# Optimization experiments

Hardware: AMD Instinct MI355X
Metric: run time of the kernel (lower is better)

The kernel has to match this reference:

```python
import jax, jax.numpy as jnp
import numpy as np

B, C, H, W = 4, 64, 128, 128
NUM_HEAD = 1
SCALE = (C // NUM_HEAD) ** (-0.5)


def setup_inputs():
    key = jax.random.key(0)
    ks = jax.random.split(key, 32)
    def nrm(k, shape, s=0.05):
        return jax.random.normal(k, shape, jnp.float32) * s
    inp = {"x": jax.random.normal(ks[0], (B, C, H, W), jnp.float32)}
    i = 1
    for wn, bn in [("Wq", "bq"), ("Wk", "bk"), ("Wv", "bv"), ("Wl", "bl"), ("Wo", "bo"), ("Wp", "bp")]:
        inp[wn] = nrm(ks[i], (C, C)); i += 1
        inp[bn] = nrm(ks[i], (C,)); i += 1
    inp["sch_dw"] = nrm(ks[i], (C, 1, 5, 1)); i += 1
    inp["sch_dwb"] = nrm(ks[i], (C,)); i += 1
    inp["sch_pw"] = nrm(ks[i], (C, C, 1, 1)); i += 1
    inp["sch_pwb"] = nrm(ks[i], (C,)); i += 1
    inp["scv_dw"] = nrm(ks[i], (C, 1, 1, 5)); i += 1
    inp["scv_dwb"] = nrm(ks[i], (C,)); i += 1
    inp["scv_pw"] = nrm(ks[i], (C, C, 1, 1)); i += 1
    inp["scv_pwb"] = nrm(ks[i], (C,)); i += 1
    inp["convh_w"] = nrm(ks[i], (C, C, 1, 1)); i += 1
    inp["convh_b"] = nrm(ks[i], (C,)); i += 1
    inp["dsc_dw"] = nrm(ks[i], (C, 1, 3, 3)); i += 1
    inp["dsc_dwb"] = nrm(ks[i], (C,)); i += 1
    inp["dsc_pw"] = nrm(ks[i], (C, C, 1, 1)); i += 1
    inp["dsc_pwb"] = nrm(ks[i], (C,)); i += 1
    inp["ln_g"] = jnp.ones((C,), jnp.float32)
    inp["ln_b"] = jnp.zeros((C,), jnp.float32)
    return inp


def _linear(x, w, b):  # x [B,N,C], w [C,C] (torch Linear convention: y = x @ w.T + b)
    return x @ w.T + b


def _dwconv(x, w, b, pad):  # depthwise: x [B,C,H,W], w [C,1,kh,kw]
    y = jax.lax.conv_general_dilated(x, w, (1, 1), [(pad[0], pad[0]), (pad[1], pad[1])],
                                     dimension_numbers=("NCHW", "OIHW", "NCHW"),
                                     feature_group_count=x.shape[1])
    return y + b[None, :, None, None]


def _pwconv(x, w, b):  # 1x1 conv: w [Co,Ci,1,1]
    return jnp.einsum("bchw,oc->bohw", x, w[:, :, 0, 0]) + b[None, :, None, None]


def _attn(q, k, v):  # [B,N,C] each; dense NxN softmax attention
    a = jax.nn.softmax(jnp.einsum("bnc,bmc->bnm", q, k) * SCALE, axis=-1)
    return jnp.einsum("bnm,bmc->bnc", a, v)


def _up2_bilinear(x):  # bilinear, scale 2, align_corners=True
    Bb, Cc, Hh, Ww = x.shape
    def coords(n):
        s = jnp.linspace(0.0, n - 1.0, 2 * n)
        i0 = jnp.floor(s).astype(jnp.int32)
        i1 = jnp.minimum(i0 + 1, n - 1)
        return i0, i1, (s - i0).astype(x.dtype)
    y0, y1, wy = coords(Hh)
    x0, x1, wx = coords(Ww)
    r = x[:, :, y0, :] * (1.0 - wy)[None, None, :, None] + x[:, :, y1, :] * wy[None, None, :, None]
    return r[:, :, :, x0] * (1.0 - wx) + r[:, :, :, x1] * wx


def _forward(x, Wq, bq, Wk, bk, Wv, bv, Wl, bl, Wo, bo, Wp, bp,
             sch_dw, sch_dwb, sch_pw, sch_pwb, scv_dw, scv_dwb, scv_pw, scv_pwb,
             convh_w, convh_b, dsc_dw, dsc_dwb, dsc_pw, dsc_pwb, ln_g, ln_b):
    Bb, Cc, Hh, Ww = x.shape
    # AvgPool2d(2,2)
    xp = x.reshape(Bb, Cc, Hh // 2, 2, Ww // 2, 2).mean((3, 5))
    Hp, Wp_ = Hh // 2, Ww // 2
    N = Hp * Wp_
    # forward_lpg: GAP-gated self-attention producing low-freq prompt
    gap = xp.mean((2, 3), keepdims=True)
    xg = (gap * xp).reshape(Bb, Cc, N).transpose(0, 2, 1)  # [B,N,C]
    q = _linear(xg, Wq, bq); k = _linear(xg, Wk, bk); v = _linear(xg, Wv, bv)
    prompt_l = _linear(_attn(q, k, v), Wl, bl).transpose(0, 2, 1).reshape(Bb, Cc, Hp, Wp_)
    # forward_hpg: separable strip-conv branches -> high-freq prompt
    x_h = _pwconv(jax.nn.gelu(_dwconv(xp, sch_dw, sch_dwb, (2, 0)), approximate=False), sch_pw, sch_pwb)
    x_v = _pwconv(jax.nn.gelu(_dwconv(xp, scv_dw, scv_dwb, (0, 2)), approximate=False), scv_pw, scv_pwb)
    prompt_h = _pwconv(x_h + x_v, convh_w, convh_b)
    # forward_pgc: cross-attention Q=high, K=low, V=linear(x)
    x_V = _linear(xp.reshape(Bb, Cc, N).transpose(0, 2, 1), Wo, bo)
    x_K = prompt_l.reshape(Bb, Cc, N).transpose(0, 2, 1)
    x_Q = prompt_h.reshape(Bb, Cc, N).transpose(0, 2, 1)
    prompt = _attn(x_Q, x_K, x_V)
    prompt = _linear(prompt, Wp, bp) + x_V
    # LayerNorm over channel dim
    mu = prompt.mean(-1, keepdims=True)
    var = jnp.mean((prompt - mu) ** 2, axis=-1, keepdims=True)
    p_norm = (prompt - mu) / jnp.sqrt(var + 1e-5) * ln_g + ln_b
    p_norm = p_norm.transpose(0, 2, 1).reshape(Bb, Cc, Hp, Wp_)
    # dsc: depthwise 3x3 -> GELU -> 1x1, residual
    out = _pwconv(jax.nn.gelu(_dwconv(p_norm, dsc_dw, dsc_dwb, (1, 1)), approximate=False), dsc_pw, dsc_pwb) + p_norm
    return _up2_bilinear(out)


def reference(x, Wq, bq, Wk, bk, Wv, bv, Wl, bl, Wo, bo, Wp, bp,
              sch_dw, sch_dwb, sch_pw, sch_pwb, scv_dw, scv_dwb, scv_pw, scv_pwb,
              convh_w, convh_b, dsc_dw, dsc_dwb, dsc_pw, dsc_pwb, ln_g, ln_b):
    return _forward(x, Wq, bq, Wk, bk, Wv, bv, Wl, bl, Wo, bo, Wp, bp,
                    sch_dw, sch_dwb, sch_pw, sch_pwb, scv_dw, scv_dwb, scv_pw, scv_pwb,
                    convh_w, convh_b, dsc_dw, dsc_dwb, dsc_pw, dsc_pwb, ln_g, ln_b)
```

## Files before the change

kernel.cpp:

```cpp
#include <hip/hip_runtime.h>
#include <math.h>

#define Bn 4
#define Cn 64
#define Np 4096
#define NSPLIT 4
#define SCALE2 0.18033688011112042f

typedef unsigned short ushort_t;
typedef __attribute__((ext_vector_type(4))) float f32x4;
typedef __attribute__((ext_vector_type(8))) short bf16x8;
typedef __attribute__((ext_vector_type(4))) short bf16x4;

__device__ __forceinline__ float gelu_exact(float x) {
    return 0.5f * x * (1.0f + erff(x * 0.70710678118654752440f));
}
__device__ __forceinline__ ushort_t f2bf(float f) {
    unsigned int u = __float_as_uint(f);
    u += 0x7fffu + ((u >> 16) & 1u);
    return (ushort_t)(u >> 16);
}
__device__ __forceinline__ ushort_t f2bf_tr(float f) {
    return (ushort_t)(__float_as_uint(f) >> 16);
}
__device__ __forceinline__ float bf2f(ushort_t h) {
    return __uint_as_float(((unsigned int)h) << 16);
}
__device__ __forceinline__ void gload_lds16(const ushort_t* g, ushort_t* l) {
    __builtin_amdgcn_global_load_lds(
        (const __attribute__((address_space(1))) void*)g,
        (__attribute__((address_space(3))) void*)l, 16, 0, 0);
}
__device__ __forceinline__ bf16x8 cvt8(const float v[8]) {
    bf16x8 r;
    #pragma unroll
    for (int j = 0; j < 8; ++j) r[j] = (short)f2bf(v[j]);
    return r;
}
__device__ __forceinline__ void gemm16(const bf16x8 af[2], const float* __restrict__ W,
                                       int l16, int quad, f32x4* acc) {
    #pragma unroll
    for (int cb = 0; cb < 4; ++cb) {
        #pragma unroll
        for (int ks = 0; ks < 2; ++ks) {
            const float* p = W + (cb * 16 + l16) * 64 + ks * 32 + quad * 8;
            float v[8];
            #pragma unroll
            for (int j = 0; j < 8; ++j) v[j] = p[j];
            acc[cb] = __builtin_amdgcn_mfma_f32_16x16x32_bf16(af[ks], cvt8(v), acc[cb], 0, 0, 0);
        }
    }
}
__device__ __forceinline__ void gemm16T(const bf16x8 af[2], const float* __restrict__ W,
                                        int l16, int quad, f32x4* acc) {
    #pragma unroll
    for (int cb = 0; cb < 4; ++cb) {
        #pragma unroll
        for (int ks = 0; ks < 2; ++ks) {
            const float* p = W + (cb * 16 + l16) * 64 + ks * 32 + quad * 8;
            float v[8];
            #pragma unroll
            for (int j = 0; j < 8; ++j) v[j] = p[j];
            acc[cb] = __builtin_amdgcn_mfma_f32_16x16x32_bf16(cvt8(v), af[ks], acc[cb], 0, 0, 0);
        }
    }
}
__device__ __forceinline__ void aload(const float* xs, int row, int quad, bf16x8 af[2]) {
    #pragma unroll
    for (int ks = 0; ks < 2; ++ks) {
        float v[8];
        #pragma unroll
        for (int j = 0; j < 8; ++j) v[j] = xs[(ks * 32 + quad * 8 + j) * 65 + row];
        af[ks] = cvt8(v);
    }
}
__device__ __forceinline__ void stage_bchw(const float* __restrict__ X, int b, int n0, int t,
                                           float* xs) {
    #pragma unroll
    for (int u = 0; u < 16; ++u) {
        int idx = t + u * 256;
        int c = idx >> 6, nl = idx & 63;
        xs[c * 65 + nl] = X[((size_t)(b * Cn + c)) * Np + n0 + nl];
    }
}
__device__ __forceinline__ void stage_comb(const ushort_t* __restrict__ OpB, const float* linv,
                                           int b, int n0, int t, float* xs) {
    const size_t SS = (size_t)Bn * Np * Cn;
    #pragma unroll
    for (int u = 0; u < 16; ++u) {
        int idx = t + u * 256;
        int nl = idx >> 6, c = idx & 63;
        size_t gi = ((size_t)(b * Np + n0 + nl)) * Cn + c;
        float s = bf2f(OpB[gi]) + bf2f(OpB[SS + gi]) +
                  bf2f(OpB[2 * SS + gi]) + bf2f(OpB[3 * SS + gi]);
        xs[c * 65 + nl] = s * linv[nl];
    }
}
__device__ __forceinline__ void store_bnc_T(ushort_t* __restrict__ Y, int b, int n, int quad,
                                            const f32x4* acc, const float* __restrict__ bias,
                                            float mult) {
    #pragma unroll
    for (int cb = 0; cb < 4; ++cb) {
        int o0 = cb * 16 + quad * 4;
        ushort4 pk;
        pk.x = f2bf((acc[cb][0] + bias[o0 + 0]) * mult);
        pk.y = f2bf((acc[cb][1] + bias[o0 + 1]) * mult);
        pk.z = f2bf((acc[cb][2] + bias[o0 + 2]) * mult);
        pk.w = f2bf((acc[cb][3] + bias[o0 + 3]) * mult);
        *(ushort4*)(Y + ((size_t)(b * Np + n)) * Cn + o0) = pk;
    }
}
__device__ __forceinline__ void store_bchw_bf16(ushort_t* __restrict__ Y, int b, int nb, int l16,
                                                const f32x4* acc, const float* __restrict__ bias) {
    #pragma unroll
    for (int cb = 0; cb < 4; ++cb) {
        int col = cb * 16 + l16;
        float bb = bias[col];
        ushort4 pk;
        pk.x = f2bf(acc[cb][0] + bb); pk.y = f2bf(acc[cb][1] + bb);
        pk.z = f2bf(acc[cb][2] + bb); pk.w = f2bf(acc[cb][3] + bb);
        *(ushort4*)(Y + ((size_t)(b * Cn + col)) * Np + nb) = pk;
    }
}

__global__ void avgpool_kernel(const float* __restrict__ x, float* __restrict__ xp,
                               float* __restrict__ gap4k,
                               const float* __restrict__ convh_w, const float* __restrict__ convh_b,
                               const float* __restrict__ sch_pw, const float* __restrict__ sch_pwb,
                               const float* __restrict__ scv_pw, const float* __restrict__ scv_pwb,
                               float* __restrict__ Wc1, float* __restrict__ Wc2,
                               float* __restrict__ bcv) {
    if (blockIdx.x < 4096) {
        int idx = blockIdx.x * 256 + threadIdx.x;
        int j  = idx & 63;
        int i  = (idx >> 6) & 63;
        int bc = idx >> 12;
        const float* p = x + ((size_t)bc * 128 + 2 * i) * 128 + 2 * j;
        float v = 0.25f * (p[0] + p[1] + p[128] + p[129]);
        xp[idx] = v;
        float s = v;
        #pragma unroll
        for (int off = 1; off < 64; off <<= 1) s += __shfl_xor(s, off, 64);
        __shared__ float sm[4];
        if ((threadIdx.x & 63) == 0) sm[threadIdx.x >> 6] = s;
        __syncthreads();
        if (threadIdx.x == 0) gap4k[blockIdx.x] = sm[0] + sm[1] + sm[2] + sm[3];
    } else {
        int g = (blockIdx.x - 4096) * 256 + threadIdx.x;
        int sel = g >> 12, idx = g & 4095;
        int o = idx >> 6, c = idx & 63;
        const float* pw = sel ? scv_pw : sch_pw;
        float acc = 0.f;
        #pragma unroll 8
        for (int m = 0; m < 64; ++m) acc += convh_w[o * 64 + m] * pw[m * 64 + c];
        (sel ? Wc2 : Wc1)[idx] = acc * SCALE2;
        if (g < 64) {
            float ab = convh_b[g];
            for (int m = 0; m < 64; ++m) ab += convh_w[g * 64 + m] * (sch_pwb[m] + scv_pwb[m]);
            bcv[g] = ab * SCALE2;
        }
    }
}

__global__ __launch_bounds__(256) void qkv_dw_kernel(
    const float* __restrict__ xp, const float* __restrict__ gap4k,
    const float* __restrict__ Wq, const float* __restrict__ bq,
    const float* __restrict__ Wk, const float* __restrict__ bk,
    const float* __restrict__ Wv, const float* __restrict__ bv,
    const float* __restrict__ Wo, const float* __restrict__ bo,
    ushort_t* __restrict__ qb, ushort_t* __restrict__ kb, ushort_t* __restrict__ vb,
    float* __restrict__ xV, ushort_t* __restrict__ xVtb,
    const float* __restrict__ wv5, const float* __restrict__ bv5,
    const float* __restrict__ wh5, const float* __restrict__ bh5,
    ushort_t* __restrict__ gh, ushort_t* __restrict__ gv) {
    int b = blockIdx.y, t = threadIdx.x;
    if (blockIdx.x >= 64) {
        int part = blockIdx.x - 64;
        int e = part * 1024 + t * 4;
        size_t base = (size_t)b * (Cn * Np) + e;
        int c = e >> 12, i = (e >> 6) & 63, j = e & 63;
        const float* p = xp + ((size_t)(b * Cn + c)) * Np;
        float accV[4], accH[4];
        #pragma unroll
        for (int k = 0; k < 4; ++k) { accV[k] = bv5[c]; accH[k] = bh5[c]; }
        #pragma unroll
        for (int d = 0; d < 5; ++d) {
            int ii = i + d - 2;
            if (ii >= 0 && ii < 64) {
                #pragma unroll
                for (int k = 0; k < 4; ++k) accV[k] += wv5[c * 5 + d] * p[ii * 64 + j + k];
            }
        }
        #pragma unroll
        for (int k = 0; k < 4; ++k) {
            #pragma unroll
            for (int d = 0; d < 5; ++d) {
                int jj = j + k + d - 2;
                if (jj >= 0 && jj < 64) accH[k] += wh5[c * 5 + d] * p[i * 64 + jj];
            }
        }
        ushort4 ph, pv_;
        ph.x = f2bf(gelu_exact(accV[0])); ph.y = f2bf(gelu_exact(accV[1]));
        ph.z = f2bf(gelu_exact(accV[2])); ph.w = f2bf(gelu_exact(accV[3]));
        pv_.x = f2bf(gelu_exact(accH[0])); pv_.y = f2bf(gelu_exact(accH[1]));
        pv_.z = f2bf(gelu_exact(accH[2])); pv_.w = f2bf(gelu_exact(accH[3]));
        *(ushort4*)(gh + base) = ph;
        *(ushort4*)(gv + base) = pv_;
        return;
    }
    __shared__ float xs[64 * 65];
    __shared__ float gl[64];
    int n0 = blockIdx.x * 64;
    int wv_ = t >> 6, lane = t & 63, l16 = lane & 15, quad = lane >> 4;
    stage_bchw(xp, b, n0, t, xs);
    if (t < 64) {
        float s = 0.f;
        #pragma unroll
        for (int u = 0; u < 16; ++u) s += gap4k[(b * 64 + t) * 16 + u];
        gl[t] = s * (1.f / 4096.f);
    }
    __syncthreads();
    int row = wv_ * 16 + l16;
    int n   = n0 + wv_ * 16 + l16;
    int nb  = n0 + wv_ * 16 + quad * 4;
    bf16x8 ar[2], ag[2];
    #pragma unroll
    for (int ks = 0; ks < 2; ++ks) {
        float vr[8], vg[8];
        #pragma unroll
        for (int j = 0; j < 8; ++j) {
            int k = ks * 32 + quad * 8 + j;
            float xv = xs[k * 65 + row];
            vr[j] = xv; vg[j] = xv * gl[k];
        }
        ar[ks] = cvt8(vr); ag[ks] = cvt8(vg);
    }
    f32x4 acc[4];
    #pragma unroll
    for (int cb = 0; cb < 4; ++cb) acc[cb] = (f32x4){0.f, 0.f, 0.f, 0.f};
    gemm16T(ag, Wq, l16, quad, acc);
    store_bnc_T(qb, b, n, quad, acc, bq, SCALE2);
    #pragma unroll
    for (int cb = 0; cb < 4; ++cb) acc[cb] = (f32x4){0.f, 0.f, 0.f, 0.f};
    gemm16T(ag, Wk, l16, quad, acc);
    store_bnc_T(kb, b, n, quad, acc, bk, 1.f);
    #pragma unroll
    for (int cb = 0; cb < 4; ++cb) acc[cb] = (f32x4){0.f, 0.f, 0.f, 0.f};
    gemm16(ag, Wv, l16, quad, acc);
    store_bchw_bf16(vb, b, nb, l16, acc, bv);
    #pragma unroll
    for (int cb = 0; cb < 4; ++cb) acc[cb] = (f32x4){0.f, 0.f, 0.f, 0.f};
    gemm16(ar, Wo, l16, quad, acc);
    #pragma unroll
    for (int cb = 0; cb < 4; ++cb) {
        int col = cb * 16 + l16;
        float bb = bo[col];
        ushort4 pk;
        float y0 = acc[cb][0] + bb, y1 = acc[cb][1] + bb, y2 = acc[cb][2] + bb, y3 = acc[cb][3] + bb;
        xV[((size_t)(b * Np + nb + 0)) * Cn + col] = y0;
        xV[((size_t)(b * Np + nb + 1)) * Cn + col] = y1;
        xV[((size_t)(b * Np + nb + 2)) * Cn + col] = y2;
        xV[((size_t)(b * Np + nb + 3)) * Cn + col] = y3;
        pk.x = f2bf(y0); pk.y = f2bf(y1); pk.z = f2bf(y2); pk.w = f2bf(y3);
        *(ushort4*)(xVtb + ((size_t)(b * Cn + col)) * Np + nb) = pk;
    }
}

__device__ __forceinline__ void attn_body(
    int xblk, int b, const ushort_t* __restrict__ Qb, const ushort_t* __restrict__ Kb,
    const ushort_t* __restrict__ Vtb, ushort_t* __restrict__ OpB, float* __restrict__ Lpart,
    ushort_t* smem) {
    ushort_t* kt0 = smem;
    ushort_t* vt0 = smem + 8192;
    int split = xblk >> 6;
    int qt    = xblk & 63;
    int n0    = qt * 64;
    int t     = threadIdx.x;
    int wave  = t >> 6, lane = t & 63;
    int l16   = lane & 15, quad = lane >> 4;

    const ushort_t* qp = Qb + ((size_t)(b * Np) + n0 + wave * 16 + l16) * Cn + quad * 8;
    bf16x8 aq0 = *(const bf16x8*)(qp);
    bf16x8 aq1 = *(const bf16x8*)(qp + 32);

    f32x4 oa[4];
    float psum = 0.f;
    #pragma unroll
    for (int db = 0; db < 4; ++db) oa[db] = (f32x4){0.f, 0.f, 0.f, 0.f};

    int lrow = lane >> 3;
    int kvbase = split * (Np / NSPLIT);
    const ushort_t* Kg = Qb == nullptr ? nullptr : Kb + ((size_t)b * Np) * Cn;
    const ushort_t* Vg = Vtb + ((size_t)b * Cn) * Np;

    auto stage = [&](int buf, int k0) {
        int wh = wave & 1;
        if (wave < 2) {
            ushort_t* dst = kt0 + buf * 4096 + wh * 2048;
            #pragma unroll
            for (int u = 0; u < 4; ++u) {
                int r = wh * 32 + u * 8 + lrow;
                int jsw = ((lane & 7) ^ lrow ^ (wh * 4 + u)) & 7;
                gload_lds16(Kg + ((size_t)(k0 + r)) * Cn + jsw * 8, dst + u * 512);
            }
        } else {
            ushort_t* dst = vt0 + buf * 4096 + wh * 2048;
            #pragma unroll
            for (int u = 0; u < 4; ++u) {
                int d = wh * 32 + u * 8 + lrow;
                int jsw = ((lane & 7) ^ lrow ^ (wh * 4 + u)) & 7;
                gload_lds16(Vg + (size_t)d * Np + k0 + jsw * 8, dst + u * 512);
            }
        }
    };
    const int NT = (Np / NSPLIT) / 64;
    stage(0, kvbase);
    __syncthreads();

    for (int m = 0; m < NT; ++m) {
        int cur = m & 1;
        if (m + 1 < NT) stage(1 - cur, kvbase + (m + 1) * 64);
        const ushort_t* ktc = kt0 + cur * 4096;
        const ushort_t* vtc = vt0 + cur * 4096;

        f32x4 sa[4];
        #pragma unroll
        for (int cb = 0; cb < 4; ++cb) sa[cb] = (f32x4){0.f, 0.f, 0.f, 0.f};
        #pragma unroll
        for (int cb = 0; cb < 4; ++cb) {
            int key = ((l16 & 7) ^ (cb * 2 + (l16 >> 3))) & 7;
            const ushort_t* krow = ktc + (cb * 16 + l16) * 64;
            bf16x8 bk0 = *(const bf16x8*)(krow + ((quad    ) ^ key) * 8);
            bf16x8 bk1 = *(const bf16x8*)(krow + ((quad + 4) ^ key) * 8);
            sa[cb] = __builtin_amdgcn_mfma_f32_16x16x32_bf16(bk0, aq0, sa[cb], 0, 0, 0);
            sa[cb] = __builtin_amdgcn_mfma_f32_16x16x32_bf16(bk1, aq1, sa[cb], 0, 0, 0);
        }
        bf16x4 pb[4];
        #pragma unroll
        for (int cb = 0; cb < 4; ++cb) {
            float p0 = exp2f(sa[cb][0]), p1 = exp2f(sa[cb][1]);
            float p2 = exp2f(sa[cb][2]), p3 = exp2f(sa[cb][3]);
            psum += (p0 + p1) + (p2 + p3);
            bf16x4 pk;
            pk[0] = (short)f2bf_tr(p0); pk[1] = (short)f2bf_tr(p1);
            pk[2] = (short)f2bf_tr(p2); pk[3] = (short)f2bf_tr(p3);
            pb[cb] = pk;
        }
        #pragma unroll
        for (int kc = 0; kc < 4; ++kc) {
            #pragma unroll
            for (int db = 0; db < 4; ++db) {
                int d = db * 16 + l16;
                int key = ((l16 & 7) ^ (db * 2 + (l16 >> 3))) & 7;
                int phys = (kc * 2 + (quad >> 1)) ^ key;
                const ushort_t* va = vtc + d * 64 + phys * 8 + (quad & 1) * 4;
                bf16x4 av = *(const bf16x4*)va;
                oa[db] = __builtin_amdgcn_mfma_f32_16x16x16bf16_1k(av, pb[kc], oa[db], 0, 0, 0);
            }
        }
        __syncthreads();
    }
    psum += __shfl_xor(psum, 16, 64);
    psum += __shfl_xor(psum, 32, 64);
    size_t obase = ((size_t)(split * Bn + b)) * Np;
    int n = n0 + wave * 16 + l16;
    if (quad == 0) Lpart[obase + n] = psum;
    #pragma unroll
    for (int db = 0; db < 4; ++db) {
        ushort4 pk;
        pk.x = f2bf(oa[db][0]); pk.y = f2bf(oa[db][1]);
        pk.z = f2bf(oa[db][2]); pk.w = f2bf(oa[db][3]);
        *(ushort4*)(OpB + (obase + n) * Cn + db * 16 + quad * 4) = pk;
    }
}

__device__ __forceinline__ void hpg_body(
    int tile, int b, const ushort_t* __restrict__ gh, const ushort_t* __restrict__ gv,
    const float* __restrict__ Wc1, const float* __restrict__ Wc2, const float* __restrict__ bcv,
    ushort_t* __restrict__ xQb, ushort_t* smem) {
    ushort_t* xs1 = smem;
    ushort_t* xs2 = smem + 4608;
    int n0 = tile * 64, t = threadIdx.x;
    int wv_ = t >> 6, lane = t & 63, l16 = lane & 15, quad = lane >> 4;
    #pragma unroll
    for (int u = 0; u < 4; ++u) {
        int lin = u * 256 + t;
        int c = lin >> 4, nl4 = (lin & 15) * 4;
        size_t gi = ((size_t)(b * Cn + c)) * Np + n0 + nl4;
        ushort4 g1 = *(const ushort4*)(gh + gi);
        ushort4 g2 = *(const ushort4*)(gv + gi);
        xs1[(nl4 + 0) * 72 + c] = g1.x; xs1[(nl4 + 1) * 72 + c] = g1.y;
        xs1[(nl4 + 2) * 72 + c] = g1.z; xs1[(nl4 + 3) * 72 + c] = g1.w;
        xs2[(nl4 + 0) * 72 + c] = g2.x; xs2[(nl4 + 1) * 72 + c] = g2.y;
        xs2[(nl4 + 2) * 72 + c] = g2.z; xs2[(nl4 + 3) * 72 + c] = g2.w;
    }
    __syncthreads();
    int row = wv_ * 16 + l16;
    bf16x8 a1[2], a2[2];
    #pragma unroll
    for (int ks = 0; ks < 2; ++ks) {
        a1[ks] = *(const bf16x8*)(xs1 + row * 72 + ks * 32 + quad * 8);
        a2[ks] = *(const bf16x8*)(xs2 + row * 72 + ks * 32 + quad * 8);
    }
    f32x4 acc[4];
    #pragma unroll
    for (int cb = 0; cb < 4; ++cb) acc[cb] = (f32x4){0.f, 0.f, 0.f, 0.f};
    gemm16T(a1, Wc1, l16, quad, acc);
    gemm16T(a2, Wc2, l16, quad, acc);
    store_bnc_T(xQb, b, n0 + wv_ * 16 + l16, quad, acc, bcv, 1.f);
}

__global__ __launch_bounds__(256) void attn_hpg_kernel(
    const ushort_t* __restrict__ Qb, const ushort_t* __restrict__ Kb,
    const ushort_t* __restrict__ Vtb, ushort_t* __restrict__ OpB, float* __restrict__ Lpart,
    const ushort_t* __restrict__ gh, const ushort_t* __restrict__ gv,
    const float* __restrict__ Wc1, const float* __restrict__ Wc2,
    const float* __restrict__ bcv, ushort_t* __restrict__ xQb) {
    __shared__ ushort_t smem[16384];
    int b = blockIdx.y;
    if (blockIdx.x < 256)
        attn_body(blockIdx.x, b, Qb, Kb, Vtb, OpB, Lpart, smem);
    else
        hpg_body(blockIdx.x - 256, b, gh, gv, Wc1, Wc2, bcv, xQb, smem);
}

__global__ __launch_bounds__(256) void wl_mfma(
    const ushort_t* __restrict__ OpB, const float* __restrict__ Lp,
    const float* __restrict__ Wl, const float* __restrict__ bl, ushort_t* __restrict__ xKb) {
    __shared__ float xs[64 * 65];
    __shared__ float linv[64];
    int b = blockIdx.y, n0 = blockIdx.x * 64, t = threadIdx.x;
    int wv_ = t >> 6, lane = t & 63, l16 = lane & 15, quad = lane >> 4;
    if (t < 64) {
        size_t li = (size_t)b * Np + n0 + t;
        const size_t LS = (size_t)Bn * Np;
        linv[t] = 1.f / (Lp[li] + Lp[LS + li] + Lp[2 * LS + li] + Lp[3 * LS + li]);
    }
    __syncthreads();
    stage_comb(OpB, linv, b, n0, t, xs);
    __syncthreads();
    bf16x8 af[2];
    aload(xs, wv_ * 16 + l16, quad, af);
    f32x4 acc[4];
    #pragma unroll
    for (int cb = 0; cb < 4; ++cb) acc[cb] = (f32x4){0.f, 0.f, 0.f, 0.f};
    gemm16T(af, Wl, l16, quad, acc);
    store_bnc_T(xKb, b, n0 + wv_ * 16 + l16, quad, acc, bl, 1.f);
}

__global__ __launch_bounds__(256) void linln_mfma(
    const ushort_t* __restrict__ OpB, const float* __restrict__ Lp,
    const float* __restrict__ Wp, const float* __restrict__ bp,
    const float* __restrict__ xV, const float* __restrict__ g, const float* __restrict__ beta,
    float* __restrict__ out) {
    __shared__ float xs[64 * 65];
    __shared__ float linv[64];
    int b = blockIdx.y, n0 = blockIdx.x * 64, t = threadIdx.x;
    int wv_ = t >> 6, lane = t & 63, l16 = lane & 15, quad = lane >> 4;
    if (t < 64) {
        size_t li = (size_t)b * Np + n0 + t;
        const size_t LS = (size_t)Bn * Np;
        linv[t] = 1.f / (Lp[li] + Lp[LS + li] + Lp[2 * LS + li] + Lp[3 * LS + li]);
    }
    __syncthreads();
    stage_comb(OpB, linv, b, n0, t, xs);
    __syncthreads();
    bf16x8 af[2];
    aload(xs, wv_ * 16 + l16, quad, af);
    f32x4 acc[4];
    #pragma unroll
    for (int cb = 0; cb < 4; ++cb) acc[cb] = (f32x4){0.f, 0.f, 0.f, 0.f};
    gemm16(af, Wp, l16, quad, acc);
    int nb = n0 + wv_ * 16 + quad * 4;
    float vals[4][4], gc[4], bec[4];
    #pragma unroll
    for (int cb = 0; cb < 4; ++cb) {
        int col = cb * 16 + l16;
        float bb = bp[col];
        gc[cb] = g[col]; bec[cb] = beta[col];
        #pragma unroll
        for (int r = 0; r < 4; ++r)
            vals[cb][r] = acc[cb][r] + bb + xV[((size_t)(b * Np + nb + r)) * Cn + col];
    }
    f32x4 yn[4];
    #pragma unroll
    for (int r = 0; r < 4; ++r) {
        float s = 0.f, s2 = 0.f;
        #pragma unroll
        for (int cb = 0; cb < 4; ++cb) { s += vals[cb][r]; s2 += vals[cb][r] * vals[cb][r]; }
        #pragma unroll
        for (int off = 1; off < 16; off <<= 1) {
            s  += __shfl_xor(s, off, 64);
            s2 += __shfl_xor(s2, off, 64);
        }
        float mu  = s * (1.f / 64.f);
        float var = s2 * (1.f / 64.f) - mu * mu;
        float ivs = rsqrtf(var + 1e-5f);
        #pragma unroll
        for (int cb = 0; cb < 4; ++cb)
            yn[cb][r] = (vals[cb][r] - mu) * ivs * gc[cb] + bec[cb];
    }
    #pragma unroll
    for (int cb = 0; cb < 4; ++cb)
        *(f32x4*)(out + ((size_t)(b * Cn + cb * 16 + l16)) * Np + nb) = yn[cb];
}

__global__ void dw3x3_gelu_kernel(const float* __restrict__ xin, const float* __restrict__ w,
                                  const float* __restrict__ bias, float* __restrict__ out) {
    int idx = blockIdx.x * 256 + threadIdx.x;
    int j = idx & 63, i = (idx >> 6) & 63, bc = idx >> 12, c = bc & 63;
    const float* p = xin + (size_t)bc * Np;
    float acc = bias[c];
    #pragma unroll
    for (int dy = 0; dy < 3; ++dy) {
        int ii = i + dy - 1;
        if (ii < 0 || ii >= 64) continue;
        #pragma unroll
        for (int dx = 0; dx < 3; ++dx) {
            int jj = j + dx - 1;
            if (jj < 0 || jj >= 64) continue;
            acc += w[c * 9 + dy * 3 + dx] * p[ii * 64 + jj];
        }
    }
    out[idx] = gelu_exact(acc);
}

__global__ __launch_bounds__(256) void dsc_mfma(
    const float* __restrict__ X, const float* __restrict__ W, const float* __restrict__ bias,
    const float* __restrict__ res, float* __restrict__ out) {
    __shared__ float xs[64 * 65];
    int b = blockIdx.y, n0 = blockIdx.x * 64, t = threadIdx.x;
    int wv_ = t >> 6, lane = t & 63, l16 = lane & 15, quad = lane >> 4;
    stage_bchw(X, b, n0, t, xs);
    __syncthreads();
    bf16x8 af[2];
    aload(xs, wv_ * 16 + l16, quad, af);
    f32x4 acc[4];
    #pragma unroll
    for (int cb = 0; cb < 4; ++cb) acc[cb] = (f32x4){0.f, 0.f, 0.f, 0.f};
    gemm16(af, W, l16, quad, acc);
    int nb = n0 + wv_ * 16 + quad * 4;
    #pragma unroll
    for (int cb = 0; cb < 4; ++cb) {
        int col = cb * 16 + l16;
        float bb = bias[col];
        size_t oi = ((size_t)(b * Cn + col)) * Np + nb;
        f32x4 rv = *(const f32x4*)(res + oi);
        f32x4 v4;
        #pragma unroll
        for (int r = 0; r < 4; ++r) v4[r] = acc[cb][r] + bb + rv[r];
        *(f32x4*)(out + oi) = v4;
    }
}

__global__ void upsample_kernel(const float* __restrict__ in, float* __restrict__ out) {
    int idx = blockIdx.x * 256 + threadIdx.x;
    int x  = idx & 127;
    int y  = (idx >> 7) & 127;
    int bc = idx >> 14;
    float sy = y * (63.f / 127.f);
    float sx = x * (63.f / 127.f);
    int y0 = (int)sy, x0 = (int)sx;
    float fy = sy - y0, fx = sx - x0;
    int y1 = min(y0 + 1, 63), x1 = min(x0 + 1, 63);
    const float* p = in + (size_t)bc * Np;
    float v00 = p[y0 * 64 + x0], v01 = p[y0 * 64 + x1];
    float v10 = p[y1 * 64 + x0], v11 = p[y1 * 64 + x1];
    out[idx] = (v00 * (1.f - fx) + v01 * fx) * (1.f - fy) +
               (v10 * (1.f - fx) + v11 * fx) * fy;
}

extern "C" void kernel_launch(void* const* d_in, const int* in_sizes, int n_in,
                              void* d_out, int out_size, void* d_ws, size_t ws_size,
                              hipStream_t stream) {
    const float* x       = (const float*)d_in[0];
    const float* Wq      = (const float*)d_in[1];
    const float* bq      = (const float*)d_in[2];
    const float* Wk      = (const float*)d_in[3];
    const float* bk      = (const float*)d_in[4];
    const float* Wv      = (const float*)d_in[5];
    const float* bv      = (const float*)d_in[6];
    const float* Wl      = (const float*)d_in[7];
    const float* bl      = (const float*)d_in[8];
    const float* Wo      = (const float*)d_in[9];
    const float* bo      = (const float*)d_in[10];
    const float* Wp      = (const float*)d_in[11];
    const float* bp      = (const float*)d_in[12];
    const float* sch_dw  = (const float*)d_in[13];
    const float* sch_dwb = (const float*)d_in[14];
    const float* sch_pw  = (const float*)d_in[15];
    const float* sch_pwb = (const float*)d_in[16];
    const float* scv_dw  = (const float*)d_in[17];
    const float* scv_dwb = (const float*)d_in[18];
    const float* scv_pw  = (const float*)d_in[19];
    const float* scv_pwb = (const float*)d_in[20];
    const float* convh_w = (const float*)d_in[21];
    const float* convh_b = (const float*)d_in[22];
    const float* dsc_dw  = (const float*)d_in[23];
    const float* dsc_dwb = (const float*)d_in[24];
    const float* dsc_pw  = (const float*)d_in[25];
    const float* dsc_pwb = (const float*)d_in[26];
    const float* ln_g    = (const float*)d_in[27];
    const float* ln_b    = (const float*)d_in[28];

    float* ws = (float*)d_ws;
    const size_t SZ = (size_t)Bn * Np * Cn;
    float* xp   = ws;
    float* xV   = ws + SZ;
    ushort_t* ghb = (ushort_t*)(ws + 2 * SZ);
    ushort_t* gh  = ghb;
    ushort_t* gv  = ghb + SZ;
    float* f2   = ws + 2 * SZ;
    ushort_t* bws  = (ushort_t*)(ws + 3 * SZ);
    ushort_t* qb   = bws;
    ushort_t* kb_  = bws + SZ;
    ushort_t* vb   = bws + 2 * SZ;
    ushort_t* xKb  = bws + 3 * SZ;
    ushort_t* xVtb = bws + 4 * SZ;
    ushort_t* xQb  = bws + 5 * SZ;
    ushort_t* OpB  = (ushort_t*)(ws + 6 * SZ);
    float* gap4k  = ws + 8 * SZ;
    float* Lpart  = gap4k + 4096;
    float* Wc1  = Lpart + (size_t)NSPLIT * Bn * Np;
    float* Wc2  = Wc1 + 4096;
    float* bcv  = Wc2 + 4096;

    dim3 g64(64, Bn);

    avgpool_kernel<<<4096 + 32, 256, 0, stream>>>(x, xp, gap4k,
                                                  convh_w, convh_b, sch_pw, sch_pwb,
                                                  scv_pw, scv_pwb, Wc1, Wc2, bcv);
    qkv_dw_kernel<<<dim3(64 + 256, Bn), 256, 0, stream>>>(
        xp, gap4k, Wq, bq, Wk, bk, Wv, bv, Wo, bo,
        qb, kb_, vb, xV, xVtb, sch_dw, sch_dwb, scv_dw, scv_dwb, gh, gv);
    attn_hpg_kernel<<<dim3(256 + 64, Bn), 256, 0, stream>>>(
        qb, kb_, vb, OpB, Lpart, gh, gv, Wc1, Wc2, bcv, xQb);
    wl_mfma<<<g64, 256, 0, stream>>>(OpB, Lpart, Wl, bl, xKb);
    attn_hpg_kernel<<<dim3(256, Bn), 256, 0, stream>>>(
        xQb, xKb, xVtb, OpB, Lpart, gh, gv, Wc1, Wc2, bcv, xQb);
    linln_mfma<<<g64, 256, 0, stream>>>(OpB, Lpart, Wp, bp, xV, ln_g, ln_b, xp);
    dw3x3_gelu_kernel<<<4096, 256, 0, stream>>>(xp, dsc_dw, dsc_dwb, xV);
    dsc_mfma<<<g64, 256, 0, stream>>>(xV, dsc_pw, dsc_pwb, xp, f2);
    upsample_kernel<<<16384, 256, 0, stream>>>(f2, (float*)d_out);
}
```

Before: 245.4 us.

## Fuse dw3x3+GELU into dsc GEMM, vectorize loads, restructure attention pipeline

Merges the depthwise 3x3 GELU conv into the pointwise MFMA kernel, so the intermediate tensor is never written or re-read and one launch is dropped. It also vectorizes the split-combine staging, the 5-tap strip convs and the bilinear upsample, which now writes four outputs per thread. The attention loop is reworked with precomputed swizzled LDS pointers, incrementing global pointers and a manually unrolled double-buffer loop. Each fused-conv block recomputes its neighbour rows from global memory, and that halo traffic is the cost of dropping the intermediate.

```diff
diff --git a/kernel.cpp b/kernel.cpp
--- a/kernel.cpp
+++ b/kernel.cpp
@@ -86,14 +86,20 @@
 __device__ __forceinline__ void stage_comb(const ushort_t* __restrict__ OpB, const float* linv,
                                            int b, int n0, int t, float* xs) {
     const size_t SS = (size_t)Bn * Np * Cn;
-    #pragma unroll
-    for (int u = 0; u < 16; ++u) {
-        int idx = t + u * 256;
-        int nl = idx >> 6, c = idx & 63;
-        size_t gi = ((size_t)(b * Np + n0 + nl)) * Cn + c;
-        float s = bf2f(OpB[gi]) + bf2f(OpB[SS + gi]) +
-                  bf2f(OpB[2 * SS + gi]) + bf2f(OpB[3 * SS + gi]);
-        xs[c * 65 + nl] = s * linv[nl];
+    int c4 = (t & 15) * 4;
+    #pragma unroll
+    for (int u = 0; u < 4; ++u) {
+        int nl = (t >> 4) + u * 16;
+        size_t gi = ((size_t)(b * Np + n0 + nl)) * Cn + c4;
+        ushort4 a0 = *(const ushort4*)(OpB + gi);
+        ushort4 a1 = *(const ushort4*)(OpB + SS + gi);
+        ushort4 a2 = *(const ushort4*)(OpB + 2 * SS + gi);
+        ushort4 a3 = *(const ushort4*)(OpB + 3 * SS + gi);
+        float li = linv[nl];
+        xs[(c4 + 0) * 65 + nl] = (bf2f(a0.x) + bf2f(a1.x) + bf2f(a2.x) + bf2f(a3.x)) * li;
+        xs[(c4 + 1) * 65 + nl] = (bf2f(a0.y) + bf2f(a1.y) + bf2f(a2.y) + bf2f(a3.y)) * li;
+        xs[(c4 + 2) * 65 + nl] = (bf2f(a0.z) + bf2f(a1.z) + bf2f(a2.z) + bf2f(a3.z)) * li;
+        xs[(c4 + 3) * 65 + nl] = (bf2f(a0.w) + bf2f(a1.w) + bf2f(a2.w) + bf2f(a3.w)) * li;
     }
 }
 __device__ __forceinline__ void store_bnc_T(ushort_t* __restrict__ Y, int b, int n, int quad,
@@ -187,17 +193,23 @@
         for (int d = 0; d < 5; ++d) {
             int ii = i + d - 2;
             if (ii >= 0 && ii < 64) {
-                #pragma unroll
-                for (int k = 0; k < 4; ++k) accV[k] += wv5[c * 5 + d] * p[ii * 64 + j + k];
+                f32x4 r = *(const f32x4*)(p + ii * 64 + j);
+                float w = wv5[c * 5 + d];
+                accV[0] += w * r[0]; accV[1] += w * r[1];
+                accV[2] += w * r[2]; accV[3] += w * r[3];
             }
         }
+        f32x4 c0 = *(const f32x4*)(p + i * 64 + j);
+        float col[8];
+        col[2] = c0[0]; col[3] = c0[1]; col[4] = c0[2]; col[5] = c0[3];
+        col[0] = (j >= 2)     ? p[i * 64 + j - 2] : 0.f;
+        col[1] = (j >= 1)     ? p[i * 64 + j - 1] : 0.f;
+        col[6] = (j + 4 < 64) ? p[i * 64 + j + 4] : 0.f;
+        col[7] = (j + 5 < 64) ? p[i * 64 + j + 5] : 0.f;
         #pragma unroll
         for (int k = 0; k < 4; ++k) {
             #pragma unroll
-            for (int d = 0; d < 5; ++d) {
-                int jj = j + k + d - 2;
-                if (jj >= 0 && jj < 64) accH[k] += wh5[c * 5 + d] * p[i * 64 + jj];
-            }
+            for (int d = 0; d < 5; ++d) accH[k] += wh5[c * 5 + d] * col[k + d];
         }
         ushort4 ph, pv_;
         ph.x = f2bf(gelu_exact(accV[0])); ph.y = f2bf(gelu_exact(accV[1]));
@@ -278,6 +290,8 @@
     int t     = threadIdx.x;
     int wave  = t >> 6, lane = t & 63;
     int l16   = lane & 15, quad = lane >> 4;
+    int lrow  = lane >> 3;
+    int kvbase = split * (Np / NSPLIT);
 
     const ushort_t* qp = Qb + ((size_t)(b * Np) + n0 + wave * 16 + l16) * Cn + quad * 8;
     bf16x8 aq0 = *(const bf16x8*)(qp);
@@ -288,50 +302,51 @@
     #pragma unroll
     for (int db = 0; db < 4; ++db) oa[db] = (f32x4){0.f, 0.f, 0.f, 0.f};
 
-    int lrow = lane >> 3;
-    int kvbase = split * (Np / NSPLIT);
-    const ushort_t* Kg = Qb == nullptr ? nullptr : Kb + ((size_t)b * Np) * Cn;
-    const ushort_t* Vg = Vtb + ((size_t)b * Cn) * Np;
-
-    auto stage = [&](int buf, int k0) {
-        int wh = wave & 1;
+    int wh  = wave & 1;
+    int jsw = ((lane & 7) ^ lrow) & 7;
+    const ushort_t* gK  = Kb + ((size_t)b * Np + kvbase + wh * 32 + lrow) * Cn + jsw * 8;
+    const ushort_t* gV0 = Vtb + ((size_t)(b * Cn) + wh * 32 + lrow) * Np + kvbase + jsw * 8;
+    const ushort_t* gV1 = gV0 + (size_t)8 * Np;
+    const ushort_t* gV2 = gV0 + (size_t)16 * Np;
+    const ushort_t* gV3 = gV0 + (size_t)24 * Np;
+    ushort_t* ldK = kt0 + wh * 2048;
+    ushort_t* ldV = vt0 + wh * 2048;
+
+    const ushort_t* kr0 = kt0 + l16 * 64 + ((quad ^ (l16 & 7)) & 7) * 8;
+    const ushort_t* kr1 = kt0 + l16 * 64 + (((quad + 4) ^ (l16 & 7)) & 7) * 8;
+    int h = quad >> 1, q1 = quad & 1, e = l16 & 7;
+    const ushort_t* vr0 = vt0 + l16 * 64 + (((0 + h) ^ e) & 7) * 8 + q1 * 4;
+    const ushort_t* vr1 = vt0 + l16 * 64 + (((2 + h) ^ e) & 7) * 8 + q1 * 4;
+    const ushort_t* vr2 = vt0 + l16 * 64 + (((4 + h) ^ e) & 7) * 8 + q1 * 4;
+    const ushort_t* vr3 = vt0 + l16 * 64 + (((6 + h) ^ e) & 7) * 8 + q1 * 4;
+
+    auto stage = [&](int buf) {
         if (wave < 2) {
-            ushort_t* dst = kt0 + buf * 4096 + wh * 2048;
-            #pragma unroll
-            for (int u = 0; u < 4; ++u) {
-                int r = wh * 32 + u * 8 + lrow;
-                int jsw = ((lane & 7) ^ lrow ^ (wh * 4 + u)) & 7;
-                gload_lds16(Kg + ((size_t)(k0 + r)) * Cn + jsw * 8, dst + u * 512);
-            }
+            ushort_t* dst = ldK + buf * 4096;
+            gload_lds16(gK,        dst);
+            gload_lds16(gK + 512,  dst + 512);
+            gload_lds16(gK + 1024, dst + 1024);
+            gload_lds16(gK + 1536, dst + 1536);
+            gK += 64 * Cn;
         } else {
-            ushort_t* dst = vt0 + buf * 4096 + wh * 2048;
-            #pragma unroll
-            for (int u = 0; u < 4; ++u) {
-                int d = wh * 32 + u * 8 + lrow;
-                int jsw = ((lane & 7) ^ lrow ^ (wh * 4 + u)) & 7;
-                gload_lds16(Vg + (size_t)d * Np + k0 + jsw * 8, dst + u * 512);
-            }
+            ushort_t* dst = ldV + buf * 4096;
+            gload_lds16(gV0, dst);
+            gload_lds16(gV1, dst + 512);
+            gload_lds16(gV2, dst + 1024);
+            gload_lds16(gV3, dst + 1536);
+            gV0 += 64; gV1 += 64; gV2 += 64; gV3 += 64;
         }
     };
-    const int NT = (Np / NSPLIT) / 64;
-    stage(0, kvbase);
-    __syncthreads();
-
-    for (int m = 0; m < NT; ++m) {
-        int cur = m & 1;
-        if (m + 1 < NT) stage(1 - cur, kvbase + (m + 1) * 64);
-        const ushort_t* ktc = kt0 + cur * 4096;
-        const ushort_t* vtc = vt0 + cur * 4096;
-
+
+    auto compute = [&](int B2) {
+        const int ko = B2 * 4096;
         f32x4 sa[4];
         #pragma unroll
         for (int cb = 0; cb < 4; ++cb) sa[cb] = (f32x4){0.f, 0.f, 0.f, 0.f};
         #pragma unroll
         for (int cb = 0; cb < 4; ++cb) {
-            int key = ((l16 & 7) ^ (cb * 2 + (l16 >> 3))) & 7;
-            const ushort_t* krow = ktc + (cb * 16 + l16) * 64;
-            bf16x8 bk0 = *(const bf16x8*)(krow + ((quad    ) ^ key) * 8);
-            bf16x8 bk1 = *(const bf16x8*)(krow + ((quad + 4) ^ key) * 8);
+            bf16x8 bk0 = *(const bf16x8*)(kr0 + ko + cb * 1024);
+            bf16x8 bk1 = *(const bf16x8*)(kr1 + ko + cb * 1024);
             sa[cb] = __builtin_amdgcn_mfma_f32_16x16x32_bf16(bk0, aq0, sa[cb], 0, 0, 0);
             sa[cb] = __builtin_amdgcn_mfma_f32_16x16x32_bf16(bk1, aq1, sa[cb], 0, 0, 0);
         }
@@ -347,19 +362,30 @@
             pb[cb] = pk;
         }
         #pragma unroll
-        for (int kc = 0; kc < 4; ++kc) {
-            #pragma unroll
-            for (int db = 0; db < 4; ++db) {
-                int d = db * 16 + l16;
-                int key = ((l16 & 7) ^ (db * 2 + (l16 >> 3))) & 7;
-                int phys = (kc * 2 + (quad >> 1)) ^ key;
-                const ushort_t* va = vtc + d * 64 + phys * 8 + (quad & 1) * 4;
-                bf16x4 av = *(const bf16x4*)va;
-                oa[db] = __builtin_amdgcn_mfma_f32_16x16x16bf16_1k(av, pb[kc], oa[db], 0, 0, 0);
-            }
+        for (int db = 0; db < 4; ++db) {
+            bf16x4 a0 = *(const bf16x4*)(vr0 + ko + db * 1024);
+            bf16x4 a1 = *(const bf16x4*)(vr1 + ko + db * 1024);
+            bf16x4 a2 = *(const bf16x4*)(vr2 + ko + db * 1024);
+            bf16x4 a3 = *(const bf16x4*)(vr3 + ko + db * 1024);
+            oa[db] = __builtin_amdgcn_mfma_f32_16x16x16bf16_1k(a0, pb[0], oa[db], 0, 0, 0);
+            oa[db] = __builtin_amdgcn_mfma_f32_16x16x16bf16_1k(a1, pb[1], oa[db], 0, 0, 0);
+            oa[db] = __builtin_amdgcn_mfma_f32_16x16x16bf16_1k(a2, pb[2], oa[db], 0, 0, 0);
+            oa[db] = __builtin_amdgcn_mfma_f32_16x16x16bf16_1k(a3, pb[3], oa[db], 0, 0, 0);
         }
         __syncthreads();
-    }
+    };
+
+    const int NT = (Np / NSPLIT) / 64;
+    stage(0);
+    __syncthreads();
+    #pragma unroll 1
+    for (int mm = 0; mm < NT / 2; ++mm) {
+        stage(1);
+        compute(0);
+        if (mm < NT / 2 - 1) stage(0);
+        compute(1);
+    }
+
     psum += __shfl_xor(psum, 16, 64);
     psum += __shfl_xor(psum, 32, 64);
     size_t obase = ((size_t)(split * Bn + b)) * Np;
@@ -505,33 +531,32 @@
         *(f32x4*)(out + ((size_t)(b * Cn + cb * 16 + l16)) * Np + nb) = yn[cb];
 }
 
-__global__ void dw3x3_gelu_kernel(const float* __restrict__ xin, const float* __restrict__ w,
-                                  const float* __restrict__ bias, float* __restrict__ out) {
-    int idx = blockIdx.x * 256 + threadIdx.x;
-    int j = idx & 63, i = (idx >> 6) & 63, bc = idx >> 12, c = bc & 63;
-    const float* p = xin + (size_t)bc * Np;
-    float acc = bias[c];
-    #pragma unroll
-    for (int dy = 0; dy < 3; ++dy) {
-        int ii = i + dy - 1;
-        if (ii < 0 || ii >= 64) continue;
-        #pragma unroll
-        for (int dx = 0; dx < 3; ++dx) {
-            int jj = j + dx - 1;
-            if (jj < 0 || jj >= 64) continue;
-            acc += w[c * 9 + dy * 3 + dx] * p[ii * 64 + jj];
-        }
-    }
-    out[idx] = gelu_exact(acc);
-}
-
 __global__ __launch_bounds__(256) void dsc_mfma(
-    const float* __restrict__ X, const float* __restrict__ W, const float* __restrict__ bias,
-    const float* __restrict__ res, float* __restrict__ out) {
+    const float* __restrict__ X, const float* __restrict__ dw, const float* __restrict__ dwb,
+    const float* __restrict__ W, const float* __restrict__ bias, float* __restrict__ out) {
     __shared__ float xs[64 * 65];
-    int b = blockIdx.y, n0 = blockIdx.x * 64, t = threadIdx.x;
+    int b = blockIdx.y, irow = blockIdx.x, n0 = irow * 64, t = threadIdx.x;
     int wv_ = t >> 6, lane = t & 63, l16 = lane & 15, quad = lane >> 4;
-    stage_bchw(X, b, n0, t, xs);
+    int j = t & 63;
+    #pragma unroll
+    for (int u = 0; u < 16; ++u) {
+        int c = (t >> 6) + u * 4;
+        const float* p = X + ((size_t)(b * Cn + c)) * Np + n0;
+        float acc = dwb[c];
+        #pragma unroll
+        for (int dy = 0; dy < 3; ++dy) {
+            int ii = irow + dy - 1;
+            if (ii < 0 || ii >= 64) continue;
+            const float* pr = p + (dy - 1) * 64;
+            #pragma unroll
+            for (int dx = 0; dx < 3; ++dx) {
+                int jj = j + dx - 1;
+                if (jj < 0 || jj >= 64) continue;
+                acc += dw[c * 9 + dy * 3 + dx] * pr[jj];
+            }
+        }
+        xs[c * 65 + j] = gelu_exact(acc);
+    }
     __syncthreads();
     bf16x8 af[2];
     aload(xs, wv_ * 16 + l16, quad, af);
@@ -545,7 +570,7 @@
         int col = cb * 16 + l16;
         float bb = bias[col];
         size_t oi = ((size_t)(b * Cn + col)) * Np + nb;
-        f32x4 rv = *(const f32x4*)(res + oi);
+        f32x4 rv = *(const f32x4*)(X + oi);
         f32x4 v4;
         #pragma unroll
         for (int r = 0; r < 4; ++r) v4[r] = acc[cb][r] + bb + rv[r];
@@ -555,19 +580,28 @@
 
 __global__ void upsample_kernel(const float* __restrict__ in, float* __restrict__ out) {
     int idx = blockIdx.x * 256 + threadIdx.x;
-    int x  = idx & 127;
-    int y  = (idx >> 7) & 127;
-    int bc = idx >> 14;
+    int x4 = (idx & 31) * 4;
+    int y  = (idx >> 5) & 127;
+    int bc = idx >> 12;
     float sy = y * (63.f / 127.f);
-    float sx = x * (63.f / 127.f);
-    int y0 = (int)sy, x0 = (int)sx;
-    float fy = sy - y0, fx = sx - x0;
-    int y1 = min(y0 + 1, 63), x1 = min(x0 + 1, 63);
-    const float* p = in + (size_t)bc * Np;
-    float v00 = p[y0 * 64 + x0], v01 = p[y0 * 64 + x1];
-    float v10 = p[y1 * 64 + x0], v11 = p[y1 * 64 + x1];
-    out[idx] = (v00 * (1.f - fx) + v01 * fx) * (1.f - fy) +
-               (v10 * (1.f - fx) + v11 * fx) * fy;
+    int y0 = (int)sy;
+    float fy = sy - y0;
+    int y1 = min(y0 + 1, 63);
+    const float* p0 = in + (size_t)bc * Np + y0 * 64;
+    const float* p1 = in + (size_t)bc * Np + y1 * 64;
+    f32x4 o;
+    #pragma unroll
+    for (int k = 0; k < 4; ++k) {
+        int xo = x4 + k;
+        float sx = xo * (63.f / 127.f);
+        int x0 = (int)sx;
+        float fx = sx - x0;
+        int x1 = min(x0 + 1, 63);
+        float r0 = p0[x0] + (p0[x1] - p0[x0]) * fx;
+        float r1 = p1[x0] + (p1[x1] - p1[x0]) * fx;
+        o[k] = r0 + (r1 - r0) * fy;
+    }
+    *(f32x4*)(out + (size_t)idx * 4) = o;
 }
 
 extern "C" void kernel_launch(void* const* d_in, const int* in_sizes, int n_in,
@@ -639,7 +673,6 @@
     attn_hpg_kernel<<<dim3(256, Bn), 256, 0, stream>>>(
         xQb, xKb, xVtb, OpB, Lpart, gh, gv, Wc1, Wc2, bcv, xQb);
     linln_mfma<<<g64, 256, 0, stream>>>(OpB, Lpart, Wp, bp, xV, ln_g, ln_b, xp);
-    dw3x3_gelu_kernel<<<4096, 256, 0, stream>>>(xp, dsc_dw, dsc_dwb, xV);
-    dsc_mfma<<<g64, 256, 0, stream>>>(xV, dsc_pw, dsc_pwb, xp, f2);
-    upsample_kernel<<<16384, 256, 0, stream>>>(f2, (float*)d_out);
-}
+    dsc_mfma<<<g64, 256, 0, stream>>>(xp, dsc_dw, dsc_dwb, dsc_pw, dsc_pwb, f2);
+    upsample_kernel<<<4096, 256, 0, stream>>>(f2, (float*)d_out);
+}
```

New measurement: 265.1 us. 8.0% more time.
